# Kernel tuning notes

Hardware: AMD Instinct MI355X
Metric: run time of the kernel (lower is better)

## Reference

```python
import jax, jax.numpy as jnp
import numpy as np

N_NODES = 100000
N_EDGES = 1000000
N_GRAPHS = 2048
IN_DIM, HIDDEN, OUT_DIM = 5, 64, 128


def setup_inputs() -> dict:
    key = jax.random.key(0)
    ks = jax.random.split(key, 12)
    x = jax.random.normal(ks[0], (N_NODES, IN_DIM), dtype=jnp.float32)
    edge_index = jax.random.randint(ks[1], (2, N_EDGES), 0, N_NODES, dtype=jnp.int64)
    batch = jnp.sort(jax.random.randint(ks[2], (N_NODES,), 0, N_GRAPHS, dtype=jnp.int64))
    def lin(k, fan_in, fan_out):
        bound = 1.0 / np.sqrt(fan_in)
        kw, kb = jax.random.split(k)
        W = jax.random.uniform(kw, (fan_in, fan_out), jnp.float32, -bound, bound)
        b = jax.random.uniform(kb, (fan_out,), jnp.float32, -bound, bound)
        return W, b
    W1, b1 = lin(ks[3], IN_DIM, HIDDEN)
    W2, b2 = lin(ks[4], HIDDEN, HIDDEN)
    W3, b3 = lin(ks[5], HIDDEN, HIDDEN)
    W4, b4 = lin(ks[6], HIDDEN, OUT_DIM)
    return {"x": x, "edge_index": edge_index, "batch": batch,
            "W1": W1, "b1": b1, "W2": W2, "b2": b2,
            "W3": W3, "b3": b3, "W4": W4, "b4": b4}


def _gcn_conv(x, W, b, src, dst, norm, n):
    # h = x W; message from src, scaled by symmetric norm, scattered to dst
    h = x @ W                                   # [N, F]
    msg = h[src] * norm[:, None]                # [E+N, F] gather
    agg = jax.ops.segment_sum(msg, dst, num_segments=n)  # scatter-add
    return agg + b


def reference(x, edge_index, batch, W1, b1, W2, b2, W3, b3, W4, b4):
    n = x.shape[0]
    loop = jnp.arange(n, dtype=edge_index.dtype)
    # GCN with self-loops: src -> dst aggregation, D^-1/2 A_hat D^-1/2 norm
    src = jnp.concatenate([edge_index[0], loop])
    dst = jnp.concatenate([edge_index[1], loop])
    deg = jax.ops.segment_sum(jnp.ones_like(dst, dtype=x.dtype), dst, num_segments=n)
    dinv = jnp.where(deg > 0, jax.lax.rsqrt(jnp.maximum(deg, 1.0)), 0.0)
    norm = dinv[src] * dinv[dst]                # [E+N]

    h = jax.nn.relu(_gcn_conv(x, W1, b1, src, dst, norm, n))
    h = jax.nn.relu(_gcn_conv(h, W2, b2, src, dst, norm, n))

    # global mean pool per graph
    sums = jax.ops.segment_sum(h, batch, num_segments=N_GRAPHS)      # [G, F]
    cnts = jax.ops.segment_sum(jnp.ones((n,), h.dtype), batch, num_segments=N_GRAPHS)
    pooled = sums / jnp.maximum(cnts, 1.0)[:, None]

    # MLP head
    z = jax.nn.relu(pooled @ W3 + b3)
    return z @ W4 + b4
```

## Files before the change

### kernel.cpp

```cpp
#include <hip/hip_runtime.h>
#include <hip/hip_fp16.h>

#define N_NODES  100000
#define N_EDGES  1000000
#define N_GRAPHS 2048
#define IN_DIM   5
#define HIDDEN   64
#define OUT_DIM  128
#define CAP      32
#define NA       512
#define PART     256
#define NBIN     391
#define LSTR     72
#define NPB      64
#define POOLG    16

typedef _Float16 f16x8 __attribute__((ext_vector_type(8)));
typedef float    f32x4 __attribute__((ext_vector_type(4)));

__global__ void k_hist(const int* __restrict__ dst, int* __restrict__ histT) {
    __shared__ int h[NBIN];
    int t = threadIdx.x, b = blockIdx.x;
    for (int i = t; i < NBIN; i += 256) h[i] = 0;
    __syncthreads();
    for (int e = b * 256 + t; e < N_EDGES; e += NA * 256)
        atomicAdd(&h[dst[e] >> 8], 1);
    __syncthreads();
    for (int i = t; i < NBIN; i += 256) histT[i * NA + b] = h[i];
}

__global__ void k_scanA(int* __restrict__ histT, int* __restrict__ total) {
    __shared__ int s[2][256];
    int bin = blockIdx.x, t = threadIdx.x;
    int* col = histT + bin * NA;
    int v0 = col[2 * t], v1 = col[2 * t + 1];
    int pair = v0 + v1;
    int cur = 0;
    s[0][t] = pair;
    __syncthreads();
    for (int off = 1; off < 256; off <<= 1) {
        int nv = s[cur][t] + ((t >= off) ? s[cur][t - off] : 0);
        s[cur ^ 1][t] = nv;
        cur ^= 1;
        __syncthreads();
    }
    int incl = s[cur][t];
    int excl = incl - pair;
    col[2 * t]     = excl;
    col[2 * t + 1] = excl + v0;
    if (t == 255) total[bin] = incl;
}

__global__ void k_scanB(const int* __restrict__ total, int* __restrict__ binBase) {
    __shared__ int s[2][512];
    int t = threadIdx.x;
    int v = (t < NBIN) ? total[t] : 0;
    int cur = 0;
    s[0][t] = v;
    __syncthreads();
    for (int off = 1; off < 512; off <<= 1) {
        int nv = s[cur][t] + ((t >= off) ? s[cur][t - off] : 0);
        s[cur ^ 1][t] = nv;
        cur ^= 1;
        __syncthreads();
    }
    if (t < NBIN) binBase[t] = s[cur][t] - v;
    if (t == NBIN - 1) binBase[NBIN] = s[cur][t];
}

__global__ void k_part(const int* __restrict__ src, const int* __restrict__ dst,
                       const int* __restrict__ histT, const int* __restrict__ binBase,
                       int* __restrict__ epart, float* __restrict__ pooled) {
    __shared__ int off[NBIN];
    int t = threadIdx.x, b = blockIdx.x;
    for (int i = b * 256 + t; i < N_GRAPHS * HIDDEN; i += NA * 256)
        pooled[i] = 0.f;
    for (int i = t; i < NBIN; i += 256)
        off[i] = binBase[i] + histT[i * NA + b];
    __syncthreads();
    for (int e = b * 256 + t; e < N_EDGES; e += NA * 256) {
        int d = dst[e];
        int pos = atomicAdd(&off[d >> 8], 1);
        epart[pos] = ((d & (PART - 1)) << 17) | src[e];
    }
}

__global__ void __launch_bounds__(256) k_build(
        const int* __restrict__ epart, const int* __restrict__ binBase,
        const float* __restrict__ x, int* __restrict__ cnt, int* __restrict__ bkt,
        float* __restrict__ dinv, __half* __restrict__ xs) {
    __shared__ int lcnt[PART];
    __shared__ int lrows[PART * CAP];
    int t = threadIdx.x, b = blockIdx.x;
    int base = b * PART;
    for (int i = t; i < PART; i += 256) lcnt[i] = 0;
    __syncthreads();
    int estart = binBase[b], eend = binBase[b + 1];
    for (int i = estart + t; i < eend; i += 256) {
        int ed = epart[i];
        int ln = ed >> 17;
        int c = atomicAdd(&lcnt[ln], 1);
        if (c < CAP) lrows[ln * CAP + c] = ed & 0x1FFFF;
    }
    __syncthreads();
    int gbase = base * CAP;
    int lim = min(PART * CAP, N_NODES * CAP - gbase);
    for (int i = t; i < lim; i += 256) bkt[gbase + i] = lrows[i];
    for (int n = t; n < PART; n += 256) {
        int g = base + n;
        if (g < N_NODES) {
            int c = lcnt[n];
            cnt[g] = c;
            float d = rsqrtf(1.0f + (float)c);
            dinv[g] = d;
#pragma unroll
            for (int k = 0; k < 8; k++)
                xs[(size_t)g * 8 + k] =
                    __float2half((k < IN_DIM) ? x[g * IN_DIM + k] * d : 0.0f);
        }
    }
}

__global__ void __launch_bounds__(256) k_g5l12(
        const int* __restrict__ cnt, const int* __restrict__ bkt,
        const __half* __restrict__ xs,
        const float* __restrict__ W1, const float* __restrict__ b1,
        const float* __restrict__ W2, const float* __restrict__ dinv,
        __half* __restrict__ hs2h) {
    __shared__ _Float16 lh1[64 * LSTR];
    __shared__ _Float16 lw2[64 * LSTR];
    __shared__ float la5[64][8];
    int tid = threadIdx.x;
    int w = tid >> 6, l = tid & 63;
    int nodeBase = blockIdx.x * 64;

#pragma unroll
    for (int i = 0; i < 16; i++) {
        int idx = tid + i * 256;
        int k = idx >> 6, n = idx & 63;
        lw2[n * LSTR + k] = (_Float16)W2[k * HIDDEN + n];
    }

    {
        int g4 = l >> 2, l4 = l & 3;
        int ln = w * 16 + g4;
        int g = nodeBase + ln;
        float accx = 0.f, accy = 0.f;
        if (g < N_NODES) {
            const __half2* XH = (const __half2*)xs;
            int len = min(cnt[g], CAP);
            const int* row = bkt + (size_t)g * CAP;
            float2 self = __half22float2(XH[(size_t)g * 4 + l4]);
            accx = self.x; accy = self.y;
            int e = 0;
            for (; e + 4 <= len; e += 4) {
                int4 ii = *(const int4*)&row[e];
                float2 v0 = __half22float2(XH[(size_t)ii.x * 4 + l4]);
                float2 v1 = __half22float2(XH[(size_t)ii.y * 4 + l4]);
                float2 v2 = __half22float2(XH[(size_t)ii.z * 4 + l4]);
                float2 v3 = __half22float2(XH[(size_t)ii.w * 4 + l4]);
                accx += (v0.x + v1.x) + (v2.x + v3.x);
                accy += (v0.y + v1.y) + (v2.y + v3.y);
            }
            for (; e < len; e++) {
                int s = row[e];
                float2 v = __half22float2(XH[(size_t)s * 4 + l4]);
                accx += v.x; accy += v.y;
            }
            float d = dinv[g];
            accx *= d; accy *= d;
        }
        la5[ln][l4 * 2]     = accx;
        la5[ln][l4 * 2 + 1] = accy;
    }

    int f = l;
    for (int i = 0; i < 16; i++) {
        int ln = w * 16 + i;
        float t1 = b1[f];
#pragma unroll
        for (int k = 0; k < IN_DIM; k++)
            t1 += la5[ln][k] * W1[k * HIDDEN + f];
        lh1[ln * LSTR + f] = (_Float16)fmaxf(t1, 0.f);
    }
    __syncthreads();

    int quad = l >> 4, m16 = l & 15;
    f32x4 acc0 = {0.f, 0.f, 0.f, 0.f};
    f32x4 acc1 = {0.f, 0.f, 0.f, 0.f};
    f32x4 acc2 = {0.f, 0.f, 0.f, 0.f};
    f32x4 acc3 = {0.f, 0.f, 0.f, 0.f};
#pragma unroll
    for (int kc = 0; kc < 2; kc++) {
        f16x8 a = *(const f16x8*)&lh1[(w * 16 + m16) * LSTR + kc * 32 + quad * 8];
        f16x8 b0 = *(const f16x8*)&lw2[(0 * 16 + m16) * LSTR + kc * 32 + quad * 8];
        f16x8 b1f = *(const f16x8*)&lw2[(1 * 16 + m16) * LSTR + kc * 32 + quad * 8];
        f16x8 b2 = *(const f16x8*)&lw2[(2 * 16 + m16) * LSTR + kc * 32 + quad * 8];
        f16x8 b3 = *(const f16x8*)&lw2[(3 * 16 + m16) * LSTR + kc * 32 + quad * 8];
        acc0 = __builtin_amdgcn_mfma_f32_16x16x32_f16(a, b0, acc0, 0, 0, 0);
        acc1 = __builtin_amdgcn_mfma_f32_16x16x32_f16(a, b1f, acc1, 0, 0, 0);
        acc2 = __builtin_amdgcn_mfma_f32_16x16x32_f16(a, b2, acc2, 0, 0, 0);
        acc3 = __builtin_amdgcn_mfma_f32_16x16x32_f16(a, b3, acc3, 0, 0, 0);
    }
#pragma unroll
    for (int i = 0; i < 4; i++) {
        int g = nodeBase + w * 16 + quad * 4 + i;
        if (g >= N_NODES) continue;
        float dv = dinv[g];
        __half* row = hs2h + (size_t)g * HIDDEN + m16;
        row[0]  = __float2half(acc0[i] * dv);
        row[16] = __float2half(acc1[i] * dv);
        row[32] = __float2half(acc2[i] * dv);
        row[48] = __float2half(acc3[i] * dv);
    }
}

__global__ void __launch_bounds__(256) k_g2agg(
        const int* __restrict__ cnt, const int* __restrict__ bkt,
        const __half* __restrict__ hs2h, const float* __restrict__ dinv,
        const int* __restrict__ batch, const float* __restrict__ b2,
        float* __restrict__ pooled) {
    __shared__ float pool[POOLG][HIDDEN];
    __shared__ int gbase_s;
    int tid = threadIdx.x;
    int grp = tid >> 3, l8 = tid & 7;
    int base = blockIdx.x * NPB;
    for (int i = tid; i < POOLG * HIDDEN; i += 256) ((float*)pool)[i] = 0.f;
    if (tid == 0) gbase_s = batch[base];
    __syncthreads();
    int gbase = gbase_s;
    const float4* H16 = (const float4*)hs2h;
    float4 b2a = ((const float4*)b2)[l8 * 2];
    float4 b2b = ((const float4*)b2)[l8 * 2 + 1];

#define ACCA(r) { const __half2* hp_ = (const __half2*)&(r);               \
        float2 u0_ = __half22float2(hp_[0]), u1_ = __half22float2(hp_[1]); \
        float2 u2_ = __half22float2(hp_[2]), u3_ = __half22float2(hp_[3]); \
        a0 += u0_.x; a1 += u0_.y; a2 += u1_.x; a3 += u1_.y;                \
        a4 += u2_.x; a5 += u2_.y; a6 += u3_.x; a7 += u3_.y; }
#define ACCC(r) { const __half2* hp_ = (const __half2*)&(r);               \
        float2 u0_ = __half22float2(hp_[0]), u1_ = __half22float2(hp_[1]); \
        float2 u2_ = __half22float2(hp_[2]), u3_ = __half22float2(hp_[3]); \
        c0 += u0_.x; c1 += u0_.y; c2 += u1_.x; c3 += u1_.y;                \
        c4 += u2_.x; c5 += u2_.y; c6 += u3_.x; c7 += u3_.y; }

    for (int ln = grp; ln < NPB; ln += 32) {
        int node = base + ln;
        if (node >= N_NODES) break;
        int len = min(cnt[node], CAP);
        const int* row = bkt + (size_t)node * CAP;
        float a0 = 0.f, a1 = 0.f, a2 = 0.f, a3 = 0.f;
        float a4 = 0.f, a5 = 0.f, a6 = 0.f, a7 = 0.f;
        float c0 = 0.f, c1 = 0.f, c2 = 0.f, c3 = 0.f;
        float c4 = 0.f, c5 = 0.f, c6 = 0.f, c7 = 0.f;
        int e = 0;
        for (; e + 8 <= len; e += 8) {
            int4 i0 = *(const int4*)&row[e];
            int4 i1 = *(const int4*)&row[e + 4];
            float4 r0 = H16[(size_t)i0.x * 8 + l8];
            float4 r1 = H16[(size_t)i0.y * 8 + l8];
            float4 r2 = H16[(size_t)i0.z * 8 + l8];
            float4 r3 = H16[(size_t)i0.w * 8 + l8];
            float4 r4 = H16[(size_t)i1.x * 8 + l8];
            float4 r5 = H16[(size_t)i1.y * 8 + l8];
            float4 r6 = H16[(size_t)i1.z * 8 + l8];
            float4 r7 = H16[(size_t)i1.w * 8 + l8];
            ACCA(r0); ACCC(r1); ACCA(r2); ACCC(r3);
            ACCA(r4); ACCC(r5); ACCA(r6); ACCC(r7);
        }
        if (e + 4 <= len) {
            int4 i0 = *(const int4*)&row[e];
            float4 r0 = H16[(size_t)i0.x * 8 + l8];
            float4 r1 = H16[(size_t)i0.y * 8 + l8];
            float4 r2 = H16[(size_t)i0.z * 8 + l8];
            float4 r3 = H16[(size_t)i0.w * 8 + l8];
            ACCA(r0); ACCC(r1); ACCA(r2); ACCC(r3);
            e += 4;
        }
        for (; e < len; e++) {
            float4 r0 = H16[(size_t)row[e] * 8 + l8];
            ACCA(r0);
        }
        {
            float4 rs = H16[(size_t)node * 8 + l8];
            ACCA(rs);
        }
        float d = dinv[node];
        float h0 = fmaxf((a0 + c0) * d + b2a.x, 0.f);
        float h1 = fmaxf((a1 + c1) * d + b2a.y, 0.f);
        float h2 = fmaxf((a2 + c2) * d + b2a.z, 0.f);
        float h3 = fmaxf((a3 + c3) * d + b2a.w, 0.f);
        float h4 = fmaxf((a4 + c4) * d + b2b.x, 0.f);
        float h5 = fmaxf((a5 + c5) * d + b2b.y, 0.f);
        float h6 = fmaxf((a6 + c6) * d + b2b.z, 0.f);
        float h7 = fmaxf((a7 + c7) * d + b2b.w, 0.f);
        int gslot = batch[node] - gbase;
        if ((unsigned)gslot < POOLG) {
            float* pp = &pool[gslot][l8 * 8];
            atomicAdd(pp + 0, h0); atomicAdd(pp + 1, h1);
            atomicAdd(pp + 2, h2); atomicAdd(pp + 3, h3);
            atomicAdd(pp + 4, h4); atomicAdd(pp + 5, h5);
            atomicAdd(pp + 6, h6); atomicAdd(pp + 7, h7);
        } else {
            float* pp = &pooled[(size_t)batch[node] * HIDDEN + l8 * 8];
            atomicAdd(pp + 0, h0); atomicAdd(pp + 1, h1);
            atomicAdd(pp + 2, h2); atomicAdd(pp + 3, h3);
            atomicAdd(pp + 4, h4); atomicAdd(pp + 5, h5);
            atomicAdd(pp + 6, h6); atomicAdd(pp + 7, h7);
        }
    }
    __syncthreads();
    int last = min(base + NPB, N_NODES) - 1;
    int span = batch[last] - gbase + 1;
    if (span > POOLG) span = POOLG;
    for (int i = tid; i < span * HIDDEN; i += 256) {
        float v = ((const float*)pool)[i];
        if (v != 0.f)
            atomicAdd(&pooled[(size_t)gbase * HIDDEN + i], v);
    }
#undef ACCA
#undef ACCC
}

__global__ void __launch_bounds__(256) k_head(
        const float* __restrict__ pooled, const int* __restrict__ batch,
        const float* __restrict__ W3, const float* __restrict__ b3,
        const float* __restrict__ W4, const float* __restrict__ b4,
        float* __restrict__ out) {
    __shared__ float p[4][HIDDEN];
    __shared__ float z[4][HIDDEN];
    __shared__ int range[5];
    int tid = threadIdx.x;
    int g0 = blockIdx.x * 4;
    if (tid < 5) {
        int v = g0 + tid;
        int lo = 0, hi = N_NODES;
        while (lo < hi) {
            int m = (lo + hi) >> 1;
            if (batch[m] < v) lo = m + 1; else hi = m;
        }
        range[tid] = lo;
    }
    __syncthreads();
    {
        int gi = tid >> 6, f = tid & 63;
        float c = (float)(range[gi + 1] - range[gi]);
        p[gi][f] = pooled[(size_t)(g0 + gi) * HIDDEN + f] / fmaxf(c, 1.f);
    }
    __syncthreads();
    {
        int gi = tid >> 6, f = tid & 63;
        float t = b3[f];
#pragma unroll 8
        for (int k = 0; k < HIDDEN; k++) t += p[gi][k] * W3[k * HIDDEN + f];
        z[gi][f] = fmaxf(t, 0.f);
    }
    __syncthreads();
    for (int i = tid; i < 4 * OUT_DIM; i += 256) {
        int gi = i >> 7, o = i & 127;
        float t = b4[o];
#pragma unroll 8
        for (int k = 0; k < HIDDEN; k++) t += z[gi][k] * W4[k * OUT_DIM + o];
        out[(size_t)(g0 + gi) * OUT_DIM + o] = t;
    }
}

extern "C" void kernel_launch(void* const* d_in, const int* in_sizes, int n_in,
                              void* d_out, int out_size, void* d_ws, size_t ws_size,
                              hipStream_t stream) {
    const float* x  = (const float*)d_in[0];
    const int*   ei = (const int*)d_in[1];
    const int*   batch = (const int*)d_in[2];
    const float* W1 = (const float*)d_in[3];
    const float* b1 = (const float*)d_in[4];
    const float* W2 = (const float*)d_in[5];
    const float* b2 = (const float*)d_in[6];
    const float* W3 = (const float*)d_in[7];
    const float* b3 = (const float*)d_in[8];
    const float* W4 = (const float*)d_in[9];
    const float* b4 = (const float*)d_in[10];
    float* out = (float*)d_out;

    const int* src = ei;
    const int* dst = ei + N_EDGES;

    char* wp = (char*)d_ws;
    auto carve = [&](size_t bytes) -> void* {
        void* p = (void*)wp;
        wp += (bytes + 255) & ~(size_t)255;
        return p;
    };
    int*    histT   = (int*)carve((size_t)NBIN * NA * sizeof(int));
    int*    total   = (int*)carve((size_t)NBIN * sizeof(int));
    int*    binBase = (int*)carve((size_t)(NBIN + 1) * sizeof(int));
    int*    cnt     = (int*)carve((size_t)N_NODES * sizeof(int));
    int*    bkt     = (int*)carve((size_t)N_NODES * CAP * sizeof(int));
    float*  dinv    = (float*)carve((size_t)N_NODES * sizeof(float));
    __half* hs2h    = (__half*)carve((size_t)N_NODES * HIDDEN * sizeof(__half));
    __half* xs      = (__half*)carve((size_t)N_NODES * 8 * sizeof(__half));
    int*    epart   = (int*)carve((size_t)N_EDGES * sizeof(int));
    float*  pooled  = (float*)carve((size_t)N_GRAPHS * HIDDEN * sizeof(float));

    k_hist<<<NA, 256, 0, stream>>>(dst, histT);
    k_scanA<<<NBIN, 256, 0, stream>>>(histT, total);
    k_scanB<<<1, 512, 0, stream>>>(total, binBase);
    k_part<<<NA, 256, 0, stream>>>(src, dst, histT, binBase, epart, pooled);
    k_build<<<NBIN, 256, 0, stream>>>(epart, binBase, x, cnt, bkt, dinv, xs);

    k_g5l12<<<(N_NODES + 63) / 64, 256, 0, stream>>>(cnt, bkt, xs, W1, b1, W2,
                                                     dinv, hs2h);
    k_g2agg<<<(N_NODES + NPB - 1) / NPB, 256, 0, stream>>>(cnt, bkt, hs2h, dinv,
                                                           batch, b2, pooled);
    k_head<<<N_GRAPHS / 4, 256, 0, stream>>>(pooled, batch, W3, b3, W4, b4, out);
}
```

Before: 188.5 us.

## Assign one block per graph for layer-2 aggregation and pooling, drop atomics

Adds a kernel that computes per-graph node ranges from the sorted batch vector. The layer-2 aggregation then runs one block per graph, accumulating pooled sums in registers and reducing them with wave shuffles and shared memory. This removes the shared and global float atomics, the pooled zero-fill, and the binary searches in the head. In exchange, blocks get uneven work because graph sizes vary (about 49 nodes each), and 32 node groups per block leave some lanes idle.

```diff
diff --git a/kernel.cpp b/kernel.cpp
--- a/kernel.cpp
+++ b/kernel.cpp
@@ -12,8 +12,6 @@
 #define PART     256
 #define NBIN     391
 #define LSTR     72
-#define NPB      64
-#define POOLG    16
 
 typedef _Float16 f16x8 __attribute__((ext_vector_type(8)));
 typedef float    f32x4 __attribute__((ext_vector_type(4)));
@@ -68,13 +66,21 @@
     if (t == NBIN - 1) binBase[NBIN] = s[cur][t];
 }
 
+__global__ void k_ranges(const int* __restrict__ batch, int* __restrict__ gs) {
+    int i = blockIdx.x * 256 + threadIdx.x;
+    if (i >= N_NODES) return;
+    int bi = batch[i];
+    int bp = (i == 0) ? -1 : batch[i - 1];
+    for (int g = bp + 1; g <= bi; g++) gs[g] = i;
+    if (i == N_NODES - 1)
+        for (int g = bi + 1; g <= N_GRAPHS; g++) gs[g] = N_NODES;
+}
+
 __global__ void k_part(const int* __restrict__ src, const int* __restrict__ dst,
                        const int* __restrict__ histT, const int* __restrict__ binBase,
-                       int* __restrict__ epart, float* __restrict__ pooled) {
+                       int* __restrict__ epart) {
     __shared__ int off[NBIN];
     int t = threadIdx.x, b = blockIdx.x;
-    for (int i = b * 256 + t; i < N_GRAPHS * HIDDEN; i += NA * 256)
-        pooled[i] = 0.f;
     for (int i = t; i < NBIN; i += 256)
         off[i] = binBase[i] + histT[i * NA + b];
     __syncthreads();
@@ -215,23 +221,21 @@
     }
 }
 
-__global__ void __launch_bounds__(256) k_g2agg(
+__global__ void __launch_bounds__(256) k_g2pool(
         const int* __restrict__ cnt, const int* __restrict__ bkt,
         const __half* __restrict__ hs2h, const float* __restrict__ dinv,
-        const int* __restrict__ batch, const float* __restrict__ b2,
+        const int* __restrict__ gs, const float* __restrict__ b2,
         float* __restrict__ pooled) {
-    __shared__ float pool[POOLG][HIDDEN];
-    __shared__ int gbase_s;
-    int tid = threadIdx.x;
+    __shared__ float pool[4][HIDDEN];
+    int g = blockIdx.x, tid = threadIdx.x;
     int grp = tid >> 3, l8 = tid & 7;
-    int base = blockIdx.x * NPB;
-    for (int i = tid; i < POOLG * HIDDEN; i += 256) ((float*)pool)[i] = 0.f;
-    if (tid == 0) gbase_s = batch[base];
-    __syncthreads();
-    int gbase = gbase_s;
+    int w = tid >> 6;
+    int s = gs[g], e = gs[g + 1];
     const float4* H16 = (const float4*)hs2h;
     float4 b2a = ((const float4*)b2)[l8 * 2];
     float4 b2b = ((const float4*)b2)[l8 * 2 + 1];
+    float p0 = 0.f, p1 = 0.f, p2 = 0.f, p3 = 0.f;
+    float p4 = 0.f, p5 = 0.f, p6 = 0.f, p7 = 0.f;
 
 #define ACCA(r) { const __half2* hp_ = (const __half2*)&(r);               \
         float2 u0_ = __half22float2(hp_[0]), u1_ = __half22float2(hp_[1]); \
@@ -244,19 +248,17 @@
         c0 += u0_.x; c1 += u0_.y; c2 += u1_.x; c3 += u1_.y;                \
         c4 += u2_.x; c5 += u2_.y; c6 += u3_.x; c7 += u3_.y; }
 
-    for (int ln = grp; ln < NPB; ln += 32) {
-        int node = base + ln;
-        if (node >= N_NODES) break;
+    for (int node = s + grp; node < e; node += 32) {
         int len = min(cnt[node], CAP);
         const int* row = bkt + (size_t)node * CAP;
         float a0 = 0.f, a1 = 0.f, a2 = 0.f, a3 = 0.f;
         float a4 = 0.f, a5 = 0.f, a6 = 0.f, a7 = 0.f;
         float c0 = 0.f, c1 = 0.f, c2 = 0.f, c3 = 0.f;
         float c4 = 0.f, c5 = 0.f, c6 = 0.f, c7 = 0.f;
-        int e = 0;
-        for (; e + 8 <= len; e += 8) {
-            int4 i0 = *(const int4*)&row[e];
-            int4 i1 = *(const int4*)&row[e + 4];
+        int ee = 0;
+        for (; ee + 8 <= len; ee += 8) {
+            int4 i0 = *(const int4*)&row[ee];
+            int4 i1 = *(const int4*)&row[ee + 4];
             float4 r0 = H16[(size_t)i0.x * 8 + l8];
             float4 r1 = H16[(size_t)i0.y * 8 + l8];
             float4 r2 = H16[(size_t)i0.z * 8 + l8];
@@ -268,17 +270,17 @@
             ACCA(r0); ACCC(r1); ACCA(r2); ACCC(r3);
             ACCA(r4); ACCC(r5); ACCA(r6); ACCC(r7);
         }
-        if (e + 4 <= len) {
-            int4 i0 = *(const int4*)&row[e];
+        if (ee + 4 <= len) {
+            int4 i0 = *(const int4*)&row[ee];
             float4 r0 = H16[(size_t)i0.x * 8 + l8];
             float4 r1 = H16[(size_t)i0.y * 8 + l8];
             float4 r2 = H16[(size_t)i0.z * 8 + l8];
             float4 r3 = H16[(size_t)i0.w * 8 + l8];
             ACCA(r0); ACCC(r1); ACCA(r2); ACCC(r3);
-            e += 4;
-        }
-        for (; e < len; e++) {
-            float4 r0 = H16[(size_t)row[e] * 8 + l8];
+            ee += 4;
+        }
+        for (; ee < len; ee++) {
+            float4 r0 = H16[(size_t)row[ee] * 8 + l8];
             ACCA(r0);
         }
         {
@@ -286,44 +288,37 @@
             ACCA(rs);
         }
         float d = dinv[node];
-        float h0 = fmaxf((a0 + c0) * d + b2a.x, 0.f);
-        float h1 = fmaxf((a1 + c1) * d + b2a.y, 0.f);
-        float h2 = fmaxf((a2 + c2) * d + b2a.z, 0.f);
-        float h3 = fmaxf((a3 + c3) * d + b2a.w, 0.f);
-        float h4 = fmaxf((a4 + c4) * d + b2b.x, 0.f);
-        float h5 = fmaxf((a5 + c5) * d + b2b.y, 0.f);
-        float h6 = fmaxf((a6 + c6) * d + b2b.z, 0.f);
-        float h7 = fmaxf((a7 + c7) * d + b2b.w, 0.f);
-        int gslot = batch[node] - gbase;
-        if ((unsigned)gslot < POOLG) {
-            float* pp = &pool[gslot][l8 * 8];
-            atomicAdd(pp + 0, h0); atomicAdd(pp + 1, h1);
-            atomicAdd(pp + 2, h2); atomicAdd(pp + 3, h3);
-            atomicAdd(pp + 4, h4); atomicAdd(pp + 5, h5);
-            atomicAdd(pp + 6, h6); atomicAdd(pp + 7, h7);
-        } else {
-            float* pp = &pooled[(size_t)batch[node] * HIDDEN + l8 * 8];
-            atomicAdd(pp + 0, h0); atomicAdd(pp + 1, h1);
-            atomicAdd(pp + 2, h2); atomicAdd(pp + 3, h3);
-            atomicAdd(pp + 4, h4); atomicAdd(pp + 5, h5);
-            atomicAdd(pp + 6, h6); atomicAdd(pp + 7, h7);
-        }
-    }
-    __syncthreads();
-    int last = min(base + NPB, N_NODES) - 1;
-    int span = batch[last] - gbase + 1;
-    if (span > POOLG) span = POOLG;
-    for (int i = tid; i < span * HIDDEN; i += 256) {
-        float v = ((const float*)pool)[i];
-        if (v != 0.f)
-            atomicAdd(&pooled[(size_t)gbase * HIDDEN + i], v);
+        p0 += fmaxf((a0 + c0) * d + b2a.x, 0.f);
+        p1 += fmaxf((a1 + c1) * d + b2a.y, 0.f);
+        p2 += fmaxf((a2 + c2) * d + b2a.z, 0.f);
+        p3 += fmaxf((a3 + c3) * d + b2a.w, 0.f);
+        p4 += fmaxf((a4 + c4) * d + b2b.x, 0.f);
+        p5 += fmaxf((a5 + c5) * d + b2b.y, 0.f);
+        p6 += fmaxf((a6 + c6) * d + b2b.z, 0.f);
+        p7 += fmaxf((a7 + c7) * d + b2b.w, 0.f);
     }
 #undef ACCA
 #undef ACCC
+#pragma unroll
+    for (int m = 8; m <= 32; m <<= 1) {
+        p0 += __shfl_xor(p0, m); p1 += __shfl_xor(p1, m);
+        p2 += __shfl_xor(p2, m); p3 += __shfl_xor(p3, m);
+        p4 += __shfl_xor(p4, m); p5 += __shfl_xor(p5, m);
+        p6 += __shfl_xor(p6, m); p7 += __shfl_xor(p7, m);
+    }
+    if ((tid & 63) < 8) {
+        float* pw = &pool[w][l8 * 8];
+        pw[0] = p0; pw[1] = p1; pw[2] = p2; pw[3] = p3;
+        pw[4] = p4; pw[5] = p5; pw[6] = p6; pw[7] = p7;
+    }
+    __syncthreads();
+    if (tid < HIDDEN)
+        pooled[(size_t)g * HIDDEN + tid] =
+            pool[0][tid] + pool[1][tid] + pool[2][tid] + pool[3][tid];
 }
 
 __global__ void __launch_bounds__(256) k_head(
-        const float* __restrict__ pooled, const int* __restrict__ batch,
+        const float* __restrict__ pooled, const int* __restrict__ gs,
         const float* __restrict__ W3, const float* __restrict__ b3,
         const float* __restrict__ W4, const float* __restrict__ b4,
         float* __restrict__ out) {
@@ -332,15 +327,7 @@
     __shared__ int range[5];
     int tid = threadIdx.x;
     int g0 = blockIdx.x * 4;
-    if (tid < 5) {
-        int v = g0 + tid;
-        int lo = 0, hi = N_NODES;
-        while (lo < hi) {
-            int m = (lo + hi) >> 1;
-            if (batch[m] < v) lo = m + 1; else hi = m;
-        }
-        range[tid] = lo;
-    }
+    if (tid < 5) range[tid] = gs[g0 + tid];
     __syncthreads();
     {
         int gi = tid >> 6, f = tid & 63;
@@ -400,16 +387,17 @@
     __half* xs      = (__half*)carve((size_t)N_NODES * 8 * sizeof(__half));
     int*    epart   = (int*)carve((size_t)N_EDGES * sizeof(int));
     float*  pooled  = (float*)carve((size_t)N_GRAPHS * HIDDEN * sizeof(float));
+    int*    gs      = (int*)carve((size_t)(N_GRAPHS + 1) * sizeof(int));
 
     k_hist<<<NA, 256, 0, stream>>>(dst, histT);
+    k_ranges<<<(N_NODES + 255) / 256, 256, 0, stream>>>(batch, gs);
     k_scanA<<<NBIN, 256, 0, stream>>>(histT, total);
     k_scanB<<<1, 512, 0, stream>>>(total, binBase);
-    k_part<<<NA, 256, 0, stream>>>(src, dst, histT, binBase, epart, pooled);
+    k_part<<<NA, 256, 0, stream>>>(src, dst, histT, binBase, epart);
     k_build<<<NBIN, 256, 0, stream>>>(epart, binBase, x, cnt, bkt, dinv, xs);
 
     k_g5l12<<<(N_NODES + 63) / 64, 256, 0, stream>>>(cnt, bkt, xs, W1, b1, W2,
                                                      dinv, hs2h);
-    k_g2agg<<<(N_NODES + NPB - 1) / NPB, 256, 0, stream>>>(cnt, bkt, hs2h, dinv,
-                                                           batch, b2, pooled);
-    k_head<<<N_GRAPHS / 4, 256, 0, stream>>>(pooled, batch, W3, b3, W4, b4, out);
-}
+    k_g2pool<<<N_GRAPHS, 256, 0, stream>>>(cnt, bkt, hs2h, dinv, gs, b2, pooled);
+    k_head<<<N_GRAPHS / 4, 256, 0, stream>>>(pooled, gs, W3, b3, W4, b4, out);
+}
```

After: 168.0 us. 1.12x faster.
